# Kernel optimization log

Hardware: AMD Instinct MI355X
Metric: run time of the kernel (lower is better)

Reference implementation:

```python
import jax, jax.numpy as jnp
import numpy as np
from jax import lax

B, S, D, H, W = 4, 4096, 512, 8, 32
LL, LG = 4, 3
HD = D // H
SF = 4   # sparsity_factor
K = 7    # depthwise conv kernel


def _ln(x, g, b):
    mu = x.mean(-1, keepdims=True)
    v = ((x - mu) ** 2).mean(-1, keepdims=True)
    return (x - mu) * lax.rsqrt(v + 1e-5) * g + b


def _mha(x, wqkv, bqkv, wp, bp, bias=None):
    Bx, Sx, Dx = x.shape
    qkv = (x @ wqkv + bqkv).reshape(Bx, Sx, 3, H, HD)
    q, k, v = jnp.moveaxis(qkv, 2, 0)          # each [B,S,H,hd]
    att = jnp.einsum('bqhd,bkhd->bhqk', q, k) * (HD ** -0.5)
    if bias is not None:
        att = att + bias                        # relative position bias [1,H,W,W]
    a = jax.nn.softmax(att, axis=-1)
    o = jnp.einsum('bhqk,bkhd->bqhd', a, v).reshape(Bx, Sx, Dx)
    return o @ wp + bp


def _ffn(x, w1, b1, w2, b2):
    return jax.nn.gelu(x @ w1 + b1) @ w2 + b2


def _dwconv(x, w, b):
    # x [B,S,D], w [D,K] depthwise, 'same' padding
    y = lax.conv_general_dilated(
        x.transpose(0, 2, 1), w[:, None, :], (1,), [((K - 1) // 2, (K - 1) // 2)],
        feature_group_count=D, dimension_numbers=('NCH', 'OIH', 'NCH'))
    return (y + b[:, None]).transpose(0, 2, 1)


def _lin_interp(x, L_out):
    # torch F.interpolate(mode='linear', align_corners=False); x [B,Lin,D]
    Lin = x.shape[1]
    pos = jnp.clip((jnp.arange(L_out, dtype=jnp.float32) + 0.5) * (Lin / L_out) - 0.5,
                   0.0, Lin - 1)
    i0 = jnp.floor(pos).astype(jnp.int32)
    i1 = jnp.minimum(i0 + 1, Lin - 1)
    w = (pos - i0)[None, :, None]
    return x[:, i0] * (1.0 - w) + x[:, i1] * w


_rel_idx = np.arange(W)[:, None] - np.arange(W)[None, :] + W - 1   # [W,W]


def _local_attn(x, wqkv, bqkv, wp, bp, rel):
    # Swin-style non-overlapping window attention with relative position bias
    NW = S // W
    bias = rel[_rel_idx].transpose(2, 0, 1)[None]   # [1,H,W,W]
    xw = x.reshape(B * NW, W, D)
    return _mha(xw, wqkv, bqkv, wp, bp, bias).reshape(B, S, D)


def _global_attn(x, wqkv, bqkv, wp, bp):
    # strided sparse global attention + linear interpolation back to S
    if S > SF * 32:
        stride = max(1, S // (SF * 32))
        xs = x[:, ::stride]                         # [B, 128, D]
        return _lin_interp(_mha(xs, wqkv, bqkv, wp, bp), S)
    return _mha(x, wqkv, bqkv, wp, bp)


def _forward(x, p):
    (lqkv_w, lqkv_b, lproj_w, lproj_b, lrel, lconv_w, lconv_b,
     ln1_g, ln1_b, lffn_w1, lffn_b1, lffn_w2, lffn_b2, ln2_g, ln2_b,
     gqkv_w, gqkv_b, gproj_w, gproj_b, gn1_g, gn1_b,
     gffn_w1, gffn_b1, gffn_w2, gffn_b2, gn2_g, gn2_b,
     fw_local, fw_global, fn_g, fn_b) = p
    # local branch: window attention + depthwise conv + FFN, pre-sum/post-norm
    xl = x
    for i in range(LL):
        a = _local_attn(xl, lqkv_w[i], lqkv_b[i], lproj_w[i], lproj_b[i], lrel[i])
        xl = _ln(xl + a, ln1_g[i], ln1_b[i])
        xl = xl + _dwconv(xl, lconv_w[i], lconv_b[i])
        f = _ffn(xl, lffn_w1[i], lffn_b1[i], lffn_w2[i], lffn_b2[i])
        xl = _ln(xl + f, ln2_g[i], ln2_b[i])
    # global branch: sparse strided attention + FFN
    xg = x
    for i in range(LG):
        a = _global_attn(xg, gqkv_w[i], gqkv_b[i], gproj_w[i], gproj_b[i])
        xg = _ln(xg + a, gn1_g[i], gn1_b[i])
        f = _ffn(xg, gffn_w1[i], gffn_b1[i], gffn_w2[i], gffn_b2[i])
        xg = _ln(xg + f, gn2_g[i], gn2_b[i])
    # weighted_sum branch fusion + LayerNorm
    w = jax.nn.softmax(jnp.stack([fw_local, fw_global]))
    return _ln(w[0] * xl + w[1] * xg, fn_g, fn_b)


def setup_inputs() -> dict:
    ks = iter(jax.random.split(jax.random.key(0), 48))
    def r(shape, s=0.02):
        return jax.random.normal(next(ks), shape, dtype=jnp.float32) * s
    return {
        'x': jax.random.normal(next(ks), (B, S, D), dtype=jnp.float32),
        'lqkv_w': r((LL, D, 3 * D)), 'lqkv_b': jnp.zeros((LL, 3 * D)),
        'lproj_w': r((LL, D, D)), 'lproj_b': jnp.zeros((LL, D)),
        'lrel': r((LL, 2 * W - 1, H)),
        'lconv_w': r((LL, D, K)), 'lconv_b': jnp.zeros((LL, D)),
        'ln1_g': jnp.ones((LL, D)), 'ln1_b': jnp.zeros((LL, D)),
        'lffn_w1': r((LL, D, 4 * D)), 'lffn_b1': jnp.zeros((LL, 4 * D)),
        'lffn_w2': r((LL, 4 * D, D)), 'lffn_b2': jnp.zeros((LL, D)),
        'ln2_g': jnp.ones((LL, D)), 'ln2_b': jnp.zeros((LL, D)),
        'gqkv_w': r((LG, D, 3 * D)), 'gqkv_b': jnp.zeros((LG, 3 * D)),
        'gproj_w': r((LG, D, D)), 'gproj_b': jnp.zeros((LG, D)),
        'gn1_g': jnp.ones((LG, D)), 'gn1_b': jnp.zeros((LG, D)),
        'gffn_w1': r((LG, D, 4 * D)), 'gffn_b1': jnp.zeros((LG, 4 * D)),
        'gffn_w2': r((LG, 4 * D, D)), 'gffn_b2': jnp.zeros((LG, D)),
        'gn2_g': jnp.ones((LG, D)), 'gn2_b': jnp.zeros((LG, D)),
        'fw_local': jnp.float32(0.5), 'fw_global': jnp.float32(0.5),
        'fn_g': jnp.ones((D,)), 'fn_b': jnp.zeros((D,)),
    }


def reference(x, lqkv_w, lqkv_b, lproj_w, lproj_b, lrel, lconv_w, lconv_b,
              ln1_g, ln1_b, lffn_w1, lffn_b1, lffn_w2, lffn_b2, ln2_g, ln2_b,
              gqkv_w, gqkv_b, gproj_w, gproj_b, gn1_g, gn1_b,
              gffn_w1, gffn_b1, gffn_w2, gffn_b2, gn2_g, gn2_b,
              fw_local, fw_global, fn_g, fn_b):
    return _forward(x, (lqkv_w, lqkv_b, lproj_w, lproj_b, lrel, lconv_w, lconv_b,
                        ln1_g, ln1_b, lffn_w1, lffn_b1, lffn_w2, lffn_b2, ln2_g, ln2_b,
                        gqkv_w, gqkv_b, gproj_w, gproj_b, gn1_g, gn1_b,
                        gffn_w1, gffn_b1, gffn_w2, gffn_b2, gn2_g, gn2_b,
                        fw_local, fw_global, fn_g, fn_b))
```

## Files before the change

### kernel.cpp

```cpp
#include <hip/hip_runtime.h>
#include <math.h>

typedef __attribute__((ext_vector_type(8))) short short8;
typedef __attribute__((ext_vector_type(4))) float float4_t;
typedef __attribute__((ext_vector_type(4))) unsigned short ushort4_t;

#define DEV static __device__ __forceinline__

DEV unsigned short f2b(float f) {
    union { float f; unsigned int u; } x; x.f = f;
    unsigned int r = x.u + 0x7fffu + ((x.u >> 16) & 1u);
    return (unsigned short)(r >> 16);
}
DEV float b2f(unsigned short u) {
    union { unsigned int u; float f; } x; x.u = ((unsigned int)u) << 16;
    return x.f;
}
DEV float gelu_f(float x) {
    float u = 0.7978845608028654f * (x + 0.044715f * x * x * x);
    float e = __expf(-2.0f * u);
    return x / (1.0f + e);
}

DEV void gld16(unsigned short* lds, const unsigned short* g) {
    __builtin_amdgcn_global_load_lds(
        (const __attribute__((address_space(1))) unsigned int*)g,
        (__attribute__((address_space(3))) unsigned int*)lds,
        16, 0, 0);
}

__global__ __launch_bounds__(256) void transpose_cast_kernel(
    const float* __restrict__ W, unsigned short* __restrict__ WT, int Kd, int Nd)
{
    __shared__ float tile[32][33];
    int n0 = blockIdx.x * 32, k0 = blockIdx.y * 32;
    int tx = threadIdx.x & 31, ty = threadIdx.x >> 5;
    #pragma unroll
    for (int r = ty; r < 32; r += 8)
        tile[r][tx] = W[(size_t)(k0 + r) * Nd + n0 + tx];
    __syncthreads();
    #pragma unroll
    for (int r = ty; r < 32; r += 8)
        WT[(size_t)(n0 + r) * Kd + k0 + tx] = f2b(tile[tx][r]);
}

__global__ __launch_bounds__(256) void copy_cast_kernel(
    const float* __restrict__ x, float* __restrict__ xl, float* __restrict__ xg,
    unsigned short* __restrict__ xb, int n)
{
    int i = blockIdx.x * 256 + threadIdx.x;
    if (i < n) { float v = x[i]; xl[i] = v; xg[i] = v; xb[i] = f2b(v); }
}

template<int BN>
__global__ __launch_bounds__(256) void gemm_db_kernel(
    const unsigned short* __restrict__ A,
    const unsigned short* __restrict__ BT,
    const float* __restrict__ bias,
    const float* __restrict__ residual,
    float* __restrict__ Cf,
    unsigned short* __restrict__ Cb,
    int M, int N, int K, int act)
{
    constexpr int NI = (BN == 128) ? 4 : 2;
    __shared__ __align__(16) unsigned short As[2][128 * 32];
    __shared__ __align__(16) unsigned short Bs[2][BN * 32];
    const int tid = threadIdx.x;
    const int wave = tid >> 6, lane = tid & 63;
    const int quad = lane >> 4, l16 = lane & 15;
    const int m0 = blockIdx.x * 128, n0 = blockIdx.y * BN;
    const int wm = (BN == 128) ? (wave >> 1) * 64 : wave * 32;
    const int wn = (BN == 128) ? (wave & 1) * 64 : 0;

    float4_t acc[NI][4] = {};

    const int lrow = lane >> 2;
    const int lcol = (lane & 3) * 8;
    const int r0 = wave * 16 + lrow;
    const unsigned short* Ag0 = A  + (size_t)(m0 + r0) * K + lcol;
    const unsigned short* Ag1 = A  + (size_t)(m0 + 64 + r0) * K + lcol;
    const unsigned short* Bg0 = BT + (size_t)(n0 + r0) * K + lcol;
    const unsigned short* Bg1 = (BN == 128) ? BT + (size_t)(n0 + 64 + r0) * K + lcol : nullptr;
    const int soff = (wave * 16) * 32 + lane * 8;

    const int iters = K >> 5;
    gld16(&As[0][soff], Ag0);
    gld16(&As[0][soff + 64 * 32], Ag1);
    gld16(&Bs[0][soff], Bg0);
    if (BN == 128) gld16(&Bs[0][soff + 64 * 32], Bg1);
    __syncthreads();

    for (int k = 0; k < iters; k++) {
        const int cur = k & 1;
        if (k + 1 < iters) {
            const int koff = (k + 1) << 5;
            const int nxt = cur ^ 1;
            gld16(&As[nxt][soff], Ag0 + koff);
            gld16(&As[nxt][soff + 64 * 32], Ag1 + koff);
            gld16(&Bs[nxt][soff], Bg0 + koff);
            if (BN == 128) gld16(&Bs[nxt][soff + 64 * 32], Bg1 + koff);
        }
        short8 a[NI], b[4];
        #pragma unroll
        for (int i = 0; i < NI; i++)
            a[i] = *(const short8*)(&As[cur][(wm + i * 16 + l16) * 32 + quad * 8]);
        #pragma unroll
        for (int j = 0; j < 4; j++)
            b[j] = *(const short8*)(&Bs[cur][(wn + j * 16 + l16) * 32 + quad * 8]);
        #pragma unroll
        for (int i = 0; i < NI; i++)
            #pragma unroll
            for (int j = 0; j < 4; j++)
                acc[i][j] = __builtin_amdgcn_mfma_f32_16x16x32_bf16(b[j], a[i], acc[i][j], 0, 0, 0);
        __syncthreads();
    }

    #pragma unroll
    for (int i = 0; i < NI; i++) {
        const int row = m0 + wm + i * 16 + l16;
        #pragma unroll
        for (int j = 0; j < 4; j++) {
            const int col = n0 + wn + j * 16 + quad * 4;
            const size_t idx = (size_t)row * N + col;
            float4_t v = acc[i][j] + *(const float4_t*)(bias + col);
            if (act == 1) {
                #pragma unroll
                for (int r = 0; r < 4; r++) v[r] = gelu_f(v[r]);
            }
            if (residual) v += *(const float4_t*)(residual + idx);
            if (Cf) *(float4_t*)(Cf + idx) = v;
            if (Cb) {
                ushort4_t o = { f2b(v[0]), f2b(v[1]), f2b(v[2]), f2b(v[3]) };
                *(ushort4_t*)(Cb + idx) = o;
            }
        }
    }
}

__global__ __launch_bounds__(256) void ln_kernel(
    const float* __restrict__ X, const float* __restrict__ g, const float* __restrict__ b,
    float* __restrict__ Yf, unsigned short* __restrict__ Yb)
{
    const int row = blockIdx.x, tid = threadIdx.x;
    const float* xr = X + (size_t)row * 512;
    float v0 = xr[tid], v1 = xr[tid + 256];
    float s = v0 + v1;
    #pragma unroll
    for (int o = 32; o > 0; o >>= 1) s += __shfl_down(s, o);
    __shared__ float red[4];
    __shared__ float stat[2];
    if ((tid & 63) == 0) red[tid >> 6] = s;
    __syncthreads();
    if (tid == 0) stat[0] = (red[0] + red[1] + red[2] + red[3]) * (1.0f / 512.0f);
    __syncthreads();
    float mu = stat[0];
    float d0 = v0 - mu, d1 = v1 - mu;
    float s2 = d0 * d0 + d1 * d1;
    #pragma unroll
    for (int o = 32; o > 0; o >>= 1) s2 += __shfl_down(s2, o);
    if ((tid & 63) == 0) red[tid >> 6] = s2;
    __syncthreads();
    if (tid == 0) stat[1] = rsqrtf((red[0] + red[1] + red[2] + red[3]) * (1.0f / 512.0f) + 1e-5f);
    __syncthreads();
    float rs = stat[1];
    float y0 = d0 * rs * g[tid] + b[tid];
    float y1 = d1 * rs * g[tid + 256] + b[tid + 256];
    if (Yf) { float* yr = Yf + (size_t)row * 512; yr[tid] = y0; yr[tid + 256] = y1; }
    if (Yb) { unsigned short* yb = Yb + (size_t)row * 512; yb[tid] = f2b(y0); yb[tid + 256] = f2b(y1); }
}

__global__ __launch_bounds__(256) void interp_ln_kernel(
    const float* __restrict__ GA, float* __restrict__ XG,
    const float* __restrict__ g, const float* __restrict__ b,
    unsigned short* __restrict__ Yb)
{
    const int row = blockIdx.x, tid = threadIdx.x;
    const int bb = row >> 12, s = row & 4095;
    float pos = (s + 0.5f) * (128.0f / 4096.0f) - 0.5f;
    pos = fminf(fmaxf(pos, 0.0f), 127.0f);
    int i0 = (int)floorf(pos);
    int i1 = min(i0 + 1, 127);
    float w = pos - (float)i0;
    const float* ga0 = GA + ((size_t)bb * 128 + i0) * 512;
    const float* ga1 = GA + ((size_t)bb * 128 + i1) * 512;
    float* xr = XG + (size_t)row * 512;
    float v0 = xr[tid]       + ga0[tid]       * (1.0f - w) + ga1[tid]       * w;
    float v1 = xr[tid + 256] + ga0[tid + 256] * (1.0f - w) + ga1[tid + 256] * w;
    float sm = v0 + v1;
    #pragma unroll
    for (int o = 32; o > 0; o >>= 1) sm += __shfl_down(sm, o);
    __shared__ float red[4];
    __shared__ float stat[2];
    if ((tid & 63) == 0) red[tid >> 6] = sm;
    __syncthreads();
    if (tid == 0) stat[0] = (red[0] + red[1] + red[2] + red[3]) * (1.0f / 512.0f);
    __syncthreads();
    float mu = stat[0];
    float d0 = v0 - mu, d1 = v1 - mu;
    float s2 = d0 * d0 + d1 * d1;
    #pragma unroll
    for (int o = 32; o > 0; o >>= 1) s2 += __shfl_down(s2, o);
    if ((tid & 63) == 0) red[tid >> 6] = s2;
    __syncthreads();
    if (tid == 0) stat[1] = rsqrtf((red[0] + red[1] + red[2] + red[3]) * (1.0f / 512.0f) + 1e-5f);
    __syncthreads();
    float rs = stat[1];
    float y0 = d0 * rs * g[tid] + b[tid];
    float y1 = d1 * rs * g[tid + 256] + b[tid + 256];
    xr[tid] = y0;           xr[tid + 256] = y1;
    unsigned short* yb = Yb + (size_t)row * 512;
    yb[tid] = f2b(y0);      yb[tid + 256] = f2b(y1);
}

__global__ __launch_bounds__(256) void local_attn_kernel(
    const unsigned short* __restrict__ QKV, const float* __restrict__ rel,
    unsigned short* __restrict__ OUT)
{
    const int blk = blockIdx.x;
    const int h = blk & 7;
    const int win = (blk >> 3) & 127;
    const int b = blk >> 10;
    const int rowbase = b * 4096 + win * 32;
    __shared__ float q[32][64], k[32][65], v[32][64];
    __shared__ float sc[32][33];
    const int tid = threadIdx.x;
    for (int idx = tid; idx < 2048; idx += 256) {
        int i = idx >> 6, d = idx & 63;
        const unsigned short* base = QKV + (size_t)(rowbase + i) * 1536 + h * 64 + d;
        q[i][d] = b2f(base[0]);
        k[i][d] = b2f(base[512]);
        v[i][d] = b2f(base[1024]);
    }
    __syncthreads();
    for (int idx = tid; idx < 1024; idx += 256) {
        int i = idx >> 5, j = idx & 31;
        float s = 0.f;
        #pragma unroll
        for (int d = 0; d < 64; d++) s += q[i][d] * k[j][d];
        sc[i][j] = s * 0.125f + rel[(i - j + 31) * 8 + h];
    }
    __syncthreads();
    if (tid < 32) {
        float mx = -1e30f;
        for (int j = 0; j < 32; j++) mx = fmaxf(mx, sc[tid][j]);
        float sum = 0.f;
        for (int j = 0; j < 32; j++) { float e = __expf(sc[tid][j] - mx); sc[tid][j] = e; sum += e; }
        float inv = 1.0f / sum;
        for (int j = 0; j < 32; j++) sc[tid][j] *= inv;
    }
    __syncthreads();
    for (int idx = tid; idx < 2048; idx += 256) {
        int i = idx >> 6, d = idx & 63;
        float o = 0.f;
        #pragma unroll
        for (int j = 0; j < 32; j++) o += sc[i][j] * v[j][d];
        OUT[(size_t)(rowbase + i) * 512 + h * 64 + d] = f2b(o);
    }
}

__global__ __launch_bounds__(256) void gather_xs_kernel(
    const float* __restrict__ XG, unsigned short* __restrict__ XSB)
{
    int i = blockIdx.x * 256 + threadIdx.x;
    if (i < 262144) {
        int d = i & 511, t = (i >> 9) & 127, b = i >> 16;
        XSB[i] = f2b(XG[((size_t)b * 4096 + t * 32) * 512 + d]);
    }
}

__global__ __launch_bounds__(256) void global_attn_kernel(
    const unsigned short* __restrict__ GQKV, unsigned short* __restrict__ GOUT)
{
    const int blk = blockIdx.x;
    const int qt = blk & 3, h = (blk >> 2) & 7, b = blk >> 5;
    __shared__ unsigned short ks[128 * 64], vs[128 * 64];
    __shared__ float qs[32 * 64];
    __shared__ float sc[32 * 128];
    const int tid = threadIdx.x;
    for (int idx = tid; idx < 128 * 64; idx += 256) {
        int j = idx >> 6, d = idx & 63;
        const unsigned short* rowp = GQKV + (size_t)(b * 128 + j) * 1536 + h * 64 + d;
        ks[idx] = rowp[512];
        vs[idx] = rowp[1024];
    }
    for (int idx = tid; idx < 32 * 64; idx += 256) {
        int i = idx >> 6, d = idx & 63;
        qs[idx] = b2f(GQKV[(size_t)(b * 128 + qt * 32 + i) * 1536 + h * 64 + d]);
    }
    __syncthreads();
    for (int idx = tid; idx < 32 * 128; idx += 256) {
        int i = idx >> 7, j = idx & 127;
        float s = 0.f;
        #pragma unroll
        for (int d = 0; d < 64; d++) s += qs[i * 64 + d] * b2f(ks[j * 64 + d]);
        sc[idx] = s * 0.125f;
    }
    __syncthreads();
    if (tid < 32) {
        float mx = -1e30f;
        for (int j = 0; j < 128; j++) mx = fmaxf(mx, sc[tid * 128 + j]);
        float sum = 0.f;
        for (int j = 0; j < 128; j++) { float e = __expf(sc[tid * 128 + j] - mx); sc[tid * 128 + j] = e; sum += e; }
        float inv = 1.0f / sum;
        for (int j = 0; j < 128; j++) sc[tid * 128 + j] *= inv;
    }
    __syncthreads();
    for (int idx = tid; idx < 32 * 64; idx += 256) {
        int i = idx >> 6, d = idx & 63;
        float o = 0.f;
        for (int j = 0; j < 128; j++) o += sc[i * 128 + j] * b2f(vs[j * 64 + d]);
        GOUT[(size_t)(b * 128 + qt * 32 + i) * 512 + h * 64 + d] = f2b(o);
    }
}

__global__ __launch_bounds__(256) void dwconv_add_kernel(
    const float* __restrict__ X, const float* __restrict__ wconv, const float* __restrict__ bconv,
    float* __restrict__ Yf, unsigned short* __restrict__ Yb)
{
    int i = blockIdx.x * 256 + threadIdx.x;
    if (i < 2097152) {
        int dv = (i & 127) * 4;
        int s = (i >> 7) & 4095;
        int b = i >> 19;
        float4_t acc = *(const float4_t*)(bconv + dv);
        #pragma unroll
        for (int t = 0; t < 7; t++) {
            int ss = s + t - 3;
            if (ss >= 0 && ss < 4096) {
                float4_t xv = *(const float4_t*)(X + ((size_t)b * 4096 + ss) * 512 + dv);
                float4_t wv = { wconv[dv * 7 + t], wconv[(dv + 1) * 7 + t],
                                wconv[(dv + 2) * 7 + t], wconv[(dv + 3) * 7 + t] };
                acc += xv * wv;
            }
        }
        size_t e = (size_t)i * 4;
        float4_t v = *(const float4_t*)(X + e) + acc;
        *(float4_t*)(Yf + e) = v;
        ushort4_t o = { f2b(v[0]), f2b(v[1]), f2b(v[2]), f2b(v[3]) };
        *(ushort4_t*)(Yb + e) = o;
    }
}

__global__ __launch_bounds__(256) void final_kernel(
    const float* __restrict__ XL, const float* __restrict__ XG,
    const float* __restrict__ fwl, const float* __restrict__ fwg,
    const float* __restrict__ g, const float* __restrict__ bb, float* __restrict__ out)
{
    const int row = blockIdx.x, tid = threadIdx.x;
    float a = fwl[0], c = fwg[0];
    float m = fmaxf(a, c);
    float ea = __expf(a - m), ec = __expf(c - m);
    float w0 = ea / (ea + ec), w1 = ec / (ea + ec);
    const float* xlr = XL + (size_t)row * 512;
    const float* xgr = XG + (size_t)row * 512;
    float v0 = w0 * xlr[tid] + w1 * xgr[tid];
    float v1 = w0 * xlr[tid + 256] + w1 * xgr[tid + 256];
    float s = v0 + v1;
    #pragma unroll
    for (int o = 32; o > 0; o >>= 1) s += __shfl_down(s, o);
    __shared__ float red[4];
    __shared__ float stat[2];
    if ((tid & 63) == 0) red[tid >> 6] = s;
    __syncthreads();
    if (tid == 0) stat[0] = (red[0] + red[1] + red[2] + red[3]) * (1.0f / 512.0f);
    __syncthreads();
    float mu = stat[0];
    float d0 = v0 - mu, d1 = v1 - mu;
    float s2 = d0 * d0 + d1 * d1;
    #pragma unroll
    for (int o = 32; o > 0; o >>= 1) s2 += __shfl_down(s2, o);
    if ((tid & 63) == 0) red[tid >> 6] = s2;
    __syncthreads();
    if (tid == 0) stat[1] = rsqrtf((red[0] + red[1] + red[2] + red[3]) * (1.0f / 512.0f) + 1e-5f);
    __syncthreads();
    float rs = stat[1];
    float* orow = out + (size_t)row * 512;
    orow[tid]       = d0 * rs * g[tid] + bb[tid];
    orow[tid + 256] = d1 * rs * g[tid + 256] + bb[tid + 256];
}

extern "C" void kernel_launch(void* const* d_in, const int* in_sizes, int n_in,
                              void* d_out, int out_size, void* d_ws, size_t ws_size,
                              hipStream_t stream)
{
    (void)in_sizes; (void)n_in; (void)out_size; (void)ws_size;
    const float* x       = (const float*)d_in[0];
    const float* lqkv_w  = (const float*)d_in[1];
    const float* lqkv_b  = (const float*)d_in[2];
    const float* lproj_w = (const float*)d_in[3];
    const float* lproj_b = (const float*)d_in[4];
    const float* lrel    = (const float*)d_in[5];
    const float* lconv_w = (const float*)d_in[6];
    const float* lconv_b = (const float*)d_in[7];
    const float* ln1_g   = (const float*)d_in[8];
    const float* ln1_b   = (const float*)d_in[9];
    const float* lffn_w1 = (const float*)d_in[10];
    const float* lffn_b1 = (const float*)d_in[11];
    const float* lffn_w2 = (const float*)d_in[12];
    const float* lffn_b2 = (const float*)d_in[13];
    const float* ln2_g   = (const float*)d_in[14];
    const float* ln2_b   = (const float*)d_in[15];
    const float* gqkv_w  = (const float*)d_in[16];
    const float* gqkv_b  = (const float*)d_in[17];
    const float* gproj_w = (const float*)d_in[18];
    const float* gproj_b = (const float*)d_in[19];
    const float* gn1_g   = (const float*)d_in[20];
    const float* gn1_b   = (const float*)d_in[21];
    const float* gffn_w1 = (const float*)d_in[22];
    const float* gffn_b1 = (const float*)d_in[23];
    const float* gffn_w2 = (const float*)d_in[24];
    const float* gffn_b2 = (const float*)d_in[25];
    const float* gn2_g   = (const float*)d_in[26];
    const float* gn2_b   = (const float*)d_in[27];
    const float* fw_local  = (const float*)d_in[28];
    const float* fw_global = (const float*)d_in[29];
    const float* fn_g    = (const float*)d_in[30];
    const float* fn_b    = (const float*)d_in[31];
    float* out = (float*)d_out;

    const int Btot = 4 * 4096;
    const int nel = Btot * 512;

    char* wsb = (char*)d_ws;
    size_t off = 0;
    auto alloc = [&](size_t bytes) -> void* {
        void* p = wsb + off;
        off = (off + bytes + 255) & ~(size_t)255;
        return p;
    };
    float*          XL   = (float*)alloc((size_t)nel * 4);
    float*          XG   = (float*)alloc((size_t)nel * 4);
    float*          TMP  = (float*)alloc((size_t)nel * 4);
    unsigned short* XBl  = (unsigned short*)alloc((size_t)nel * 2);
    unsigned short* XBg  = (unsigned short*)alloc((size_t)nel * 2);
    unsigned short* AOUT = (unsigned short*)alloc((size_t)nel * 2);
    unsigned short* BIG  = (unsigned short*)alloc((size_t)Btot * 2048 * 2);
    unsigned short* WT   = (unsigned short*)alloc((size_t)22020096 * 2);
    unsigned short* XSB  = (unsigned short*)alloc((size_t)512 * 512 * 2);
    unsigned short* GQKV = (unsigned short*)alloc((size_t)512 * 1536 * 2);
    unsigned short* GOUT = (unsigned short*)alloc((size_t)512 * 512 * 2);
    float*          GA   = (float*)alloc((size_t)512 * 512 * 4);

    const size_t perL = 3145728;
    auto transpose = [&](const float* W_, unsigned short* WT_, int Kd, int Nd) {
        dim3 g(Nd / 32, Kd / 32);
        transpose_cast_kernel<<<g, dim3(256), 0, stream>>>(W_, WT_, Kd, Nd);
    };
    for (int i = 0; i < 4; i++) {
        unsigned short* base = WT + (size_t)i * perL;
        transpose(lqkv_w  + (size_t)i * 512 * 1536, base,                         512, 1536);
        transpose(lproj_w + (size_t)i * 512 * 512,  base + 786432,                512, 512);
        transpose(lffn_w1 + (size_t)i * 512 * 2048, base + 786432 + 262144,       512, 2048);
        transpose(lffn_w2 + (size_t)i * 2048 * 512, base + 786432 + 262144 + 1048576, 2048, 512);
    }
    for (int i = 0; i < 3; i++) {
        unsigned short* base = WT + (size_t)(4 + i) * perL;
        transpose(gqkv_w  + (size_t)i * 512 * 1536, base,                         512, 1536);
        transpose(gproj_w + (size_t)i * 512 * 512,  base + 786432,                512, 512);
        transpose(gffn_w1 + (size_t)i * 512 * 2048, base + 786432 + 262144,       512, 2048);
        transpose(gffn_w2 + (size_t)i * 2048 * 512, base + 786432 + 262144 + 1048576, 2048, 512);
    }

    copy_cast_kernel<<<dim3(nel / 256), dim3(256), 0, stream>>>(x, XL, XG, XBl, nel);

    auto gemm = [&](const unsigned short* A_, const unsigned short* BT_, const float* bias_,
                    const float* res_, float* Cf_, unsigned short* Cb_,
                    int M_, int N_, int K_, int act_) {
        if (N_ >= 1024) {
            dim3 g(M_ / 128, N_ / 128);
            gemm_db_kernel<128><<<g, dim3(256), 0, stream>>>(A_, BT_, bias_, res_, Cf_, Cb_, M_, N_, K_, act_);
        } else {
            dim3 g(M_ / 128, N_ / 64);
            gemm_db_kernel<64><<<g, dim3(256), 0, stream>>>(A_, BT_, bias_, res_, Cf_, Cb_, M_, N_, K_, act_);
        }
    };

    for (int i = 0; i < 4; i++) {
        unsigned short* base  = WT + (size_t)i * perL;
        unsigned short* qkvT  = base;
        unsigned short* projT = base + 786432;
        unsigned short* w1T   = base + 786432 + 262144;
        unsigned short* w2T   = base + 786432 + 262144 + 1048576;

        gemm(XBl, qkvT, lqkv_b + i * 1536, nullptr, nullptr, BIG, Btot, 1536, 512, 0);
        local_attn_kernel<<<dim3(4096), dim3(256), 0, stream>>>(BIG, lrel + (size_t)i * 63 * 8, AOUT);
        gemm(AOUT, projT, lproj_b + i * 512, XL, TMP, nullptr, Btot, 512, 512, 0);
        ln_kernel<<<dim3(Btot), dim3(256), 0, stream>>>(TMP, ln1_g + i * 512, ln1_b + i * 512, XL, (unsigned short*)nullptr);
        dwconv_add_kernel<<<dim3(nel / 1024), dim3(256), 0, stream>>>(XL, lconv_w + (size_t)i * 512 * 7, lconv_b + i * 512, TMP, XBl);
        gemm(XBl, w1T, lffn_b1 + i * 2048, nullptr, nullptr, BIG, Btot, 2048, 512, 1);
        gemm(BIG, w2T, lffn_b2 + i * 512, TMP, TMP, nullptr, Btot, 512, 2048, 0);
        ln_kernel<<<dim3(Btot), dim3(256), 0, stream>>>(TMP, ln2_g + i * 512, ln2_b + i * 512, XL, XBl);
    }

    for (int i = 0; i < 3; i++) {
        unsigned short* base  = WT + (size_t)(4 + i) * perL;
        unsigned short* qkvT  = base;
        unsigned short* projT = base + 786432;
        unsigned short* w1T   = base + 786432 + 262144;
        unsigned short* w2T   = base + 786432 + 262144 + 1048576;

        gather_xs_kernel<<<dim3(1024), dim3(256), 0, stream>>>(XG, XSB);
        gemm(XSB, qkvT, gqkv_b + i * 1536, nullptr, nullptr, GQKV, 512, 1536, 512, 0);
        global_attn_kernel<<<dim3(128), dim3(256), 0, stream>>>(GQKV, GOUT);
        gemm(GOUT, projT, gproj_b + i * 512, nullptr, GA, nullptr, 512, 512, 512, 0);
        interp_ln_kernel<<<dim3(Btot), dim3(256), 0, stream>>>(GA, XG, gn1_g + i * 512, gn1_b + i * 512, XBg);
        gemm(XBg, w1T, gffn_b1 + i * 2048, nullptr, nullptr, BIG, Btot, 2048, 512, 1);
        gemm(BIG, w2T, gffn_b2 + i * 512, XG, TMP, nullptr, Btot, 512, 2048, 0);
        ln_kernel<<<dim3(Btot), dim3(256), 0, stream>>>(TMP, gn2_g + i * 512, gn2_b + i * 512, XG, XBg);
    }

    final_kernel<<<dim3(Btot), dim3(256), 0, stream>>>(XL, XG, fw_local, fw_global, fn_g, fn_b, out);
}
```

Baseline: 2.246 ms.

## Vectorize elementwise kernels, wave-per-row layernorm, batch weight transposes, cheaper GELU

LayerNorm, interp-LN and final kernels now process one row per wavefront with float4 loads and shuffle-only reductions, which removes the shared-memory barriers. Copy, gather and all bf16 stores are vectorized with packed bf16x2 conversion. The weight transposes are batched into four launches over a z-dimension instead of 28 separate launches. Local attention is restructured to use vector loads, a per-row shuffle softmax and 8-wide output accumulation. GELU uses an exp2/rcp form, and the GEMM gains an occupancy hint, which could raise register pressure.

```diff
diff --git a/kernel.cpp b/kernel.cpp
--- a/kernel.cpp
+++ b/kernel.cpp
@@ -1,9 +1,11 @@
 #include <hip/hip_runtime.h>
+#include <hip/hip_bf16.h>
 #include <math.h>
 
 typedef __attribute__((ext_vector_type(8))) short short8;
 typedef __attribute__((ext_vector_type(4))) float float4_t;
-typedef __attribute__((ext_vector_type(4))) unsigned short ushort4_t;
+typedef __attribute__((ext_vector_type(4))) unsigned int uint4_t;
+typedef __attribute__((ext_vector_type(2))) unsigned int uint2_t;
 
 #define DEV static __device__ __forceinline__
 
@@ -16,10 +18,17 @@
     union { unsigned int u; float f; } x; x.u = ((unsigned int)u) << 16;
     return x.f;
 }
+DEV unsigned int f2b2(float lo, float hi) {
+    union { __hip_bfloat162 h; unsigned int u; } c;
+    c.h = __float22bfloat162_rn(make_float2(lo, hi));
+    return c.u;
+}
 DEV float gelu_f(float x) {
-    float u = 0.7978845608028654f * (x + 0.044715f * x * x * x);
-    float e = __expf(-2.0f * u);
-    return x / (1.0f + e);
+    const float a = -2.3022082f, b = -0.10294372f;
+    float x2 = x * x;
+    float p = __builtin_fmaf(x2, b, a);
+    float e = __builtin_amdgcn_exp2f(p * x);
+    return x * __builtin_amdgcn_rcpf(1.0f + e);
 }
 
 DEV void gld16(unsigned short* lds, const unsigned short* g) {
@@ -29,9 +38,14 @@
         16, 0, 0);
 }
 
-__global__ __launch_bounds__(256) void transpose_cast_kernel(
-    const float* __restrict__ W, unsigned short* __restrict__ WT, int Kd, int Nd)
-{
+__global__ __launch_bounds__(256) void transpose_cast_batch_kernel(
+    const float* __restrict__ srcL, const float* __restrict__ srcG, int nl,
+    unsigned short* __restrict__ dst0, size_t perL, int Kd, int Nd)
+{
+    const int z = blockIdx.z;
+    const float* W = (z < nl) ? srcL + (size_t)z * Kd * Nd
+                              : srcG + (size_t)(z - nl) * Kd * Nd;
+    unsigned short* WT = dst0 + (size_t)z * perL;
     __shared__ float tile[32][33];
     int n0 = blockIdx.x * 32, k0 = blockIdx.y * 32;
     int tx = threadIdx.x & 31, ty = threadIdx.x >> 5;
@@ -46,14 +60,20 @@
 
 __global__ __launch_bounds__(256) void copy_cast_kernel(
     const float* __restrict__ x, float* __restrict__ xl, float* __restrict__ xg,
-    unsigned short* __restrict__ xb, int n)
+    unsigned short* __restrict__ xb, int n4)
 {
     int i = blockIdx.x * 256 + threadIdx.x;
-    if (i < n) { float v = x[i]; xl[i] = v; xg[i] = v; xb[i] = f2b(v); }
+    if (i < n4) {
+        float4_t v = ((const float4_t*)x)[i];
+        ((float4_t*)xl)[i] = v;
+        ((float4_t*)xg)[i] = v;
+        uint2_t p = { f2b2(v[0], v[1]), f2b2(v[2], v[3]) };
+        ((uint2_t*)xb)[i] = p;
+    }
 }
 
 template<int BN>
-__global__ __launch_bounds__(256) void gemm_db_kernel(
+__global__ __launch_bounds__(256, 3) void gemm_db_kernel(
     const unsigned short* __restrict__ A,
     const unsigned short* __restrict__ BT,
     const float* __restrict__ bias,
@@ -130,8 +150,8 @@
             if (residual) v += *(const float4_t*)(residual + idx);
             if (Cf) *(float4_t*)(Cf + idx) = v;
             if (Cb) {
-                ushort4_t o = { f2b(v[0]), f2b(v[1]), f2b(v[2]), f2b(v[3]) };
-                *(ushort4_t*)(Cb + idx) = o;
+                uint2_t o = { f2b2(v[0], v[1]), f2b2(v[2], v[3]) };
+                *(uint2_t*)(Cb + idx) = o;
             }
         }
     }
@@ -141,32 +161,37 @@
     const float* __restrict__ X, const float* __restrict__ g, const float* __restrict__ b,
     float* __restrict__ Yf, unsigned short* __restrict__ Yb)
 {
-    const int row = blockIdx.x, tid = threadIdx.x;
-    const float* xr = X + (size_t)row * 512;
-    float v0 = xr[tid], v1 = xr[tid + 256];
-    float s = v0 + v1;
-    #pragma unroll
-    for (int o = 32; o > 0; o >>= 1) s += __shfl_down(s, o);
-    __shared__ float red[4];
-    __shared__ float stat[2];
-    if ((tid & 63) == 0) red[tid >> 6] = s;
-    __syncthreads();
-    if (tid == 0) stat[0] = (red[0] + red[1] + red[2] + red[3]) * (1.0f / 512.0f);
-    __syncthreads();
-    float mu = stat[0];
-    float d0 = v0 - mu, d1 = v1 - mu;
-    float s2 = d0 * d0 + d1 * d1;
-    #pragma unroll
-    for (int o = 32; o > 0; o >>= 1) s2 += __shfl_down(s2, o);
-    if ((tid & 63) == 0) red[tid >> 6] = s2;
-    __syncthreads();
-    if (tid == 0) stat[1] = rsqrtf((red[0] + red[1] + red[2] + red[3]) * (1.0f / 512.0f) + 1e-5f);
-    __syncthreads();
-    float rs = stat[1];
-    float y0 = d0 * rs * g[tid] + b[tid];
-    float y1 = d1 * rs * g[tid + 256] + b[tid + 256];
-    if (Yf) { float* yr = Yf + (size_t)row * 512; yr[tid] = y0; yr[tid + 256] = y1; }
-    if (Yb) { unsigned short* yb = Yb + (size_t)row * 512; yb[tid] = f2b(y0); yb[tid + 256] = f2b(y1); }
+    const int row = blockIdx.x * 4 + (threadIdx.x >> 6);
+    const int lane = threadIdx.x & 63;
+    const float* xr = X + (size_t)row * 512 + lane * 8;
+    float4_t v0 = *(const float4_t*)(xr);
+    float4_t v1 = *(const float4_t*)(xr + 4);
+    float s = v0[0] + v0[1] + v0[2] + v0[3] + v1[0] + v1[1] + v1[2] + v1[3];
+    #pragma unroll
+    for (int m = 32; m > 0; m >>= 1) s += __shfl_xor(s, m);
+    float mu = s * (1.0f / 512.0f);
+    float4_t d0 = v0 - mu, d1 = v1 - mu;
+    float s2 = d0[0]*d0[0] + d0[1]*d0[1] + d0[2]*d0[2] + d0[3]*d0[3]
+             + d1[0]*d1[0] + d1[1]*d1[1] + d1[2]*d1[2] + d1[3]*d1[3];
+    #pragma unroll
+    for (int m = 32; m > 0; m >>= 1) s2 += __shfl_xor(s2, m);
+    float rs = rsqrtf(s2 * (1.0f / 512.0f) + 1e-5f);
+    float4_t g0 = *(const float4_t*)(g + lane * 8);
+    float4_t g1 = *(const float4_t*)(g + lane * 8 + 4);
+    float4_t b0 = *(const float4_t*)(b + lane * 8);
+    float4_t b1 = *(const float4_t*)(b + lane * 8 + 4);
+    float4_t y0 = d0 * rs * g0 + b0;
+    float4_t y1 = d1 * rs * g1 + b1;
+    if (Yf) {
+        float* yr = Yf + (size_t)row * 512 + lane * 8;
+        *(float4_t*)(yr) = y0;
+        *(float4_t*)(yr + 4) = y1;
+    }
+    if (Yb) {
+        uint4_t pk = { f2b2(y0[0], y0[1]), f2b2(y0[2], y0[3]),
+                       f2b2(y1[0], y1[1]), f2b2(y1[2], y1[3]) };
+        *(uint4_t*)(Yb + (size_t)row * 512 + lane * 8) = pk;
+    }
 }
 
 __global__ __launch_bounds__(256) void interp_ln_kernel(
@@ -174,42 +199,40 @@
     const float* __restrict__ g, const float* __restrict__ b,
     unsigned short* __restrict__ Yb)
 {
-    const int row = blockIdx.x, tid = threadIdx.x;
-    const int bb = row >> 12, s = row & 4095;
-    float pos = (s + 0.5f) * (128.0f / 4096.0f) - 0.5f;
+    const int row = blockIdx.x * 4 + (threadIdx.x >> 6);
+    const int lane = threadIdx.x & 63;
+    const int bb = row >> 12, sfull = row & 4095;
+    float pos = (sfull + 0.5f) * (128.0f / 4096.0f) - 0.5f;
     pos = fminf(fmaxf(pos, 0.0f), 127.0f);
     int i0 = (int)floorf(pos);
     int i1 = min(i0 + 1, 127);
     float w = pos - (float)i0;
-    const float* ga0 = GA + ((size_t)bb * 128 + i0) * 512;
-    const float* ga1 = GA + ((size_t)bb * 128 + i1) * 512;
-    float* xr = XG + (size_t)row * 512;
-    float v0 = xr[tid]       + ga0[tid]       * (1.0f - w) + ga1[tid]       * w;
-    float v1 = xr[tid + 256] + ga0[tid + 256] * (1.0f - w) + ga1[tid + 256] * w;
-    float sm = v0 + v1;
-    #pragma unroll
-    for (int o = 32; o > 0; o >>= 1) sm += __shfl_down(sm, o);
-    __shared__ float red[4];
-    __shared__ float stat[2];
-    if ((tid & 63) == 0) red[tid >> 6] = sm;
-    __syncthreads();
-    if (tid == 0) stat[0] = (red[0] + red[1] + red[2] + red[3]) * (1.0f / 512.0f);
-    __syncthreads();
-    float mu = stat[0];
-    float d0 = v0 - mu, d1 = v1 - mu;
-    float s2 = d0 * d0 + d1 * d1;
-    #pragma unroll
-    for (int o = 32; o > 0; o >>= 1) s2 += __shfl_down(s2, o);
-    if ((tid & 63) == 0) red[tid >> 6] = s2;
-    __syncthreads();
-    if (tid == 0) stat[1] = rsqrtf((red[0] + red[1] + red[2] + red[3]) * (1.0f / 512.0f) + 1e-5f);
-    __syncthreads();
-    float rs = stat[1];
-    float y0 = d0 * rs * g[tid] + b[tid];
-    float y1 = d1 * rs * g[tid + 256] + b[tid + 256];
-    xr[tid] = y0;           xr[tid + 256] = y1;
-    unsigned short* yb = Yb + (size_t)row * 512;
-    yb[tid] = f2b(y0);      yb[tid + 256] = f2b(y1);
+    const float* ga0 = GA + ((size_t)bb * 128 + i0) * 512 + lane * 8;
+    const float* ga1 = GA + ((size_t)bb * 128 + i1) * 512 + lane * 8;
+    float* xr = XG + (size_t)row * 512 + lane * 8;
+    float4_t v0 = *(const float4_t*)(xr)     + *(const float4_t*)(ga0)     * (1.0f - w) + *(const float4_t*)(ga1)     * w;
+    float4_t v1 = *(const float4_t*)(xr + 4) + *(const float4_t*)(ga0 + 4) * (1.0f - w) + *(const float4_t*)(ga1 + 4) * w;
+    float s = v0[0] + v0[1] + v0[2] + v0[3] + v1[0] + v1[1] + v1[2] + v1[3];
+    #pragma unroll
+    for (int m = 32; m > 0; m >>= 1) s += __shfl_xor(s, m);
+    float mu = s * (1.0f / 512.0f);
+    float4_t d0 = v0 - mu, d1 = v1 - mu;
+    float s2 = d0[0]*d0[0] + d0[1]*d0[1] + d0[2]*d0[2] + d0[3]*d0[3]
+             + d1[0]*d1[0] + d1[1]*d1[1] + d1[2]*d1[2] + d1[3]*d1[3];
+    #pragma unroll
+    for (int m = 32; m > 0; m >>= 1) s2 += __shfl_xor(s2, m);
+    float rs = rsqrtf(s2 * (1.0f / 512.0f) + 1e-5f);
+    float4_t g0 = *(const float4_t*)(g + lane * 8);
+    float4_t g1 = *(const float4_t*)(g + lane * 8 + 4);
+    float4_t b0 = *(const float4_t*)(b + lane * 8);
+    float4_t b1 = *(const float4_t*)(b + lane * 8 + 4);
+    float4_t y0 = d0 * rs * g0 + b0;
+    float4_t y1 = d1 * rs * g1 + b1;
+    *(float4_t*)(xr) = y0;
+    *(float4_t*)(xr + 4) = y1;
+    uint4_t pk = { f2b2(y0[0], y0[1]), f2b2(y0[2], y0[3]),
+                   f2b2(y1[0], y1[1]), f2b2(y1[2], y1[3]) };
+    *(uint4_t*)(Yb + (size_t)row * 512 + lane * 8) = pk;
 }
 
 __global__ __launch_bounds__(256) void local_attn_kernel(
@@ -224,47 +247,64 @@
     __shared__ float q[32][64], k[32][65], v[32][64];
     __shared__ float sc[32][33];
     const int tid = threadIdx.x;
-    for (int idx = tid; idx < 2048; idx += 256) {
-        int i = idx >> 6, d = idx & 63;
-        const unsigned short* base = QKV + (size_t)(rowbase + i) * 1536 + h * 64 + d;
-        q[i][d] = b2f(base[0]);
-        k[i][d] = b2f(base[512]);
-        v[i][d] = b2f(base[1024]);
-    }
-    __syncthreads();
-    for (int idx = tid; idx < 1024; idx += 256) {
-        int i = idx >> 5, j = idx & 31;
+    const int i = tid >> 3, c = tid & 7;
+    {
+        const unsigned short* base = QKV + (size_t)(rowbase + i) * 1536 + h * 64 + c * 8;
+        short8 qv = *(const short8*)(base);
+        short8 kv = *(const short8*)(base + 512);
+        short8 vv = *(const short8*)(base + 1024);
+        #pragma unroll
+        for (int r = 0; r < 8; r++) {
+            q[i][c * 8 + r] = b2f((unsigned short)qv[r]);
+            k[i][c * 8 + r] = b2f((unsigned short)kv[r]);
+            v[i][c * 8 + r] = b2f((unsigned short)vv[r]);
+        }
+    }
+    __syncthreads();
+    #pragma unroll
+    for (int p = 0; p < 4; p++) {
+        int idx = tid + p * 256;
+        int si = idx >> 5, sj = idx & 31;
         float s = 0.f;
         #pragma unroll
-        for (int d = 0; d < 64; d++) s += q[i][d] * k[j][d];
-        sc[i][j] = s * 0.125f + rel[(i - j + 31) * 8 + h];
-    }
-    __syncthreads();
-    if (tid < 32) {
-        float mx = -1e30f;
-        for (int j = 0; j < 32; j++) mx = fmaxf(mx, sc[tid][j]);
-        float sum = 0.f;
-        for (int j = 0; j < 32; j++) { float e = __expf(sc[tid][j] - mx); sc[tid][j] = e; sum += e; }
+        for (int d = 0; d < 64; d++) s += q[si][d] * k[sj][d];
+        sc[si][sj] = s * 0.125f + rel[(si - sj + 31) * 8 + h];
+    }
+    __syncthreads();
+    {
+        const int j0 = c * 4;
+        float a0 = sc[i][j0], a1 = sc[i][j0 + 1], a2 = sc[i][j0 + 2], a3 = sc[i][j0 + 3];
+        float mx = fmaxf(fmaxf(a0, a1), fmaxf(a2, a3));
+        #pragma unroll
+        for (int m = 1; m < 8; m <<= 1) mx = fmaxf(mx, __shfl_xor(mx, m));
+        float e0 = __expf(a0 - mx), e1 = __expf(a1 - mx), e2 = __expf(a2 - mx), e3 = __expf(a3 - mx);
+        float sum = e0 + e1 + e2 + e3;
+        #pragma unroll
+        for (int m = 1; m < 8; m <<= 1) sum += __shfl_xor(sum, m);
         float inv = 1.0f / sum;
-        for (int j = 0; j < 32; j++) sc[tid][j] *= inv;
-    }
-    __syncthreads();
-    for (int idx = tid; idx < 2048; idx += 256) {
-        int i = idx >> 6, d = idx & 63;
-        float o = 0.f;
-        #pragma unroll
-        for (int j = 0; j < 32; j++) o += sc[i][j] * v[j][d];
-        OUT[(size_t)(rowbase + i) * 512 + h * 64 + d] = f2b(o);
-    }
+        sc[i][j0] = e0 * inv; sc[i][j0 + 1] = e1 * inv; sc[i][j0 + 2] = e2 * inv; sc[i][j0 + 3] = e3 * inv;
+    }
+    __syncthreads();
+    float o[8] = {};
+    #pragma unroll
+    for (int j = 0; j < 32; j++) {
+        float a = sc[i][j];
+        #pragma unroll
+        for (int r = 0; r < 8; r++) o[r] += a * v[j][c * 8 + r];
+    }
+    uint4_t pk = { f2b2(o[0], o[1]), f2b2(o[2], o[3]), f2b2(o[4], o[5]), f2b2(o[6], o[7]) };
+    *(uint4_t*)(OUT + (size_t)(rowbase + i) * 512 + h * 64 + c * 8) = pk;
 }
 
 __global__ __launch_bounds__(256) void gather_xs_kernel(
     const float* __restrict__ XG, unsigned short* __restrict__ XSB)
 {
     int i = blockIdx.x * 256 + threadIdx.x;
-    if (i < 262144) {
-        int d = i & 511, t = (i >> 9) & 127, b = i >> 16;
-        XSB[i] = f2b(XG[((size_t)b * 4096 + t * 32) * 512 + d]);
+    if (i < 65536) {
+        int dv = (i & 127) * 4, t = (i >> 7) & 127, b = i >> 14;
+        float4_t v = *(const float4_t*)(XG + ((size_t)b * 4096 + t * 32) * 512 + dv);
+        uint2_t p = { f2b2(v[0], v[1]), f2b2(v[2], v[3]) };
+        *(uint2_t*)(XSB + (size_t)i * 4) = p;
     }
 }
 
@@ -336,8 +376,8 @@
         size_t e = (size_t)i * 4;
         float4_t v = *(const float4_t*)(X + e) + acc;
         *(float4_t*)(Yf + e) = v;
-        ushort4_t o = { f2b(v[0]), f2b(v[1]), f2b(v[2]), f2b(v[3]) };
-        *(ushort4_t*)(Yb + e) = o;
+        uint2_t o = { f2b2(v[0], v[1]), f2b2(v[2], v[3]) };
+        *(uint2_t*)(Yb + e) = o;
     }
 }
 
@@ -346,37 +386,33 @@
     const float* __restrict__ fwl, const float* __restrict__ fwg,
     const float* __restrict__ g, const float* __restrict__ bb, float* __restrict__ out)
 {
-    const int row = blockIdx.x, tid = threadIdx.x;
-    float a = fwl[0], c = fwg[0];
-    float m = fmaxf(a, c);
-    float ea = __expf(a - m), ec = __expf(c - m);
+    const int row = blockIdx.x * 4 + (threadIdx.x >> 6);
+    const int lane = threadIdx.x & 63;
+    float a = fwl[0], cc = fwg[0];
+    float m = fmaxf(a, cc);
+    float ea = __expf(a - m), ec = __expf(cc - m);
     float w0 = ea / (ea + ec), w1 = ec / (ea + ec);
-    const float* xlr = XL + (size_t)row * 512;
-    const float* xgr = XG + (size_t)row * 512;
-    float v0 = w0 * xlr[tid] + w1 * xgr[tid];
-    float v1 = w0 * xlr[tid + 256] + w1 * xgr[tid + 256];
-    float s = v0 + v1;
-    #pragma unroll
-    for (int o = 32; o > 0; o >>= 1) s += __shfl_down(s, o);
-    __shared__ float red[4];
-    __shared__ float stat[2];
-    if ((tid & 63) == 0) red[tid >> 6] = s;
-    __syncthreads();
-    if (tid == 0) stat[0] = (red[0] + red[1] + red[2] + red[3]) * (1.0f / 512.0f);
-    __syncthreads();
-    float mu = stat[0];
-    float d0 = v0 - mu, d1 = v1 - mu;
-    float s2 = d0 * d0 + d1 * d1;
-    #pragma unroll
-    for (int o = 32; o > 0; o >>= 1) s2 += __shfl_down(s2, o);
-    if ((tid & 63) == 0) red[tid >> 6] = s2;
-    __syncthreads();
-    if (tid == 0) stat[1] = rsqrtf((red[0] + red[1] + red[2] + red[3]) * (1.0f / 512.0f) + 1e-5f);
-    __syncthreads();
-    float rs = stat[1];
-    float* orow = out + (size_t)row * 512;
-    orow[tid]       = d0 * rs * g[tid] + bb[tid];
-    orow[tid + 256] = d1 * rs * g[tid + 256] + bb[tid + 256];
+    const float* xlr = XL + (size_t)row * 512 + lane * 8;
+    const float* xgr = XG + (size_t)row * 512 + lane * 8;
+    float4_t v0 = *(const float4_t*)(xlr)     * w0 + *(const float4_t*)(xgr)     * w1;
+    float4_t v1 = *(const float4_t*)(xlr + 4) * w0 + *(const float4_t*)(xgr + 4) * w1;
+    float s = v0[0] + v0[1] + v0[2] + v0[3] + v1[0] + v1[1] + v1[2] + v1[3];
+    #pragma unroll
+    for (int mm = 32; mm > 0; mm >>= 1) s += __shfl_xor(s, mm);
+    float mu = s * (1.0f / 512.0f);
+    float4_t d0 = v0 - mu, d1 = v1 - mu;
+    float s2 = d0[0]*d0[0] + d0[1]*d0[1] + d0[2]*d0[2] + d0[3]*d0[3]
+             + d1[0]*d1[0] + d1[1]*d1[1] + d1[2]*d1[2] + d1[3]*d1[3];
+    #pragma unroll
+    for (int mm = 32; mm > 0; mm >>= 1) s2 += __shfl_xor(s2, mm);
+    float rs = rsqrtf(s2 * (1.0f / 512.0f) + 1e-5f);
+    float4_t g0 = *(const float4_t*)(g + lane * 8);
+    float4_t g1 = *(const float4_t*)(g + lane * 8 + 4);
+    float4_t b0 = *(const float4_t*)(bb + lane * 8);
+    float4_t b1 = *(const float4_t*)(bb + lane * 8 + 4);
+    float* orow = out + (size_t)row * 512 + lane * 8;
+    *(float4_t*)(orow)     = d0 * rs * g0 + b0;
+    *(float4_t*)(orow + 4) = d1 * rs * g1 + b1;
 }
 
 extern "C" void kernel_launch(void* const* d_in, const int* in_sizes, int n_in,
@@ -442,26 +478,19 @@
     float*          GA   = (float*)alloc((size_t)512 * 512 * 4);
 
     const size_t perL = 3145728;
-    auto transpose = [&](const float* W_, unsigned short* WT_, int Kd, int Nd) {
-        dim3 g(Nd / 32, Kd / 32);
-        transpose_cast_kernel<<<g, dim3(256), 0, stream>>>(W_, WT_, Kd, Nd);
-    };
-    for (int i = 0; i < 4; i++) {
-        unsigned short* base = WT + (size_t)i * perL;
-        transpose(lqkv_w  + (size_t)i * 512 * 1536, base,                         512, 1536);
-        transpose(lproj_w + (size_t)i * 512 * 512,  base + 786432,                512, 512);
-        transpose(lffn_w1 + (size_t)i * 512 * 2048, base + 786432 + 262144,       512, 2048);
-        transpose(lffn_w2 + (size_t)i * 2048 * 512, base + 786432 + 262144 + 1048576, 2048, 512);
-    }
-    for (int i = 0; i < 3; i++) {
-        unsigned short* base = WT + (size_t)(4 + i) * perL;
-        transpose(gqkv_w  + (size_t)i * 512 * 1536, base,                         512, 1536);
-        transpose(gproj_w + (size_t)i * 512 * 512,  base + 786432,                512, 512);
-        transpose(gffn_w1 + (size_t)i * 512 * 2048, base + 786432 + 262144,       512, 2048);
-        transpose(gffn_w2 + (size_t)i * 2048 * 512, base + 786432 + 262144 + 1048576, 2048, 512);
-    }
-
-    copy_cast_kernel<<<dim3(nel / 256), dim3(256), 0, stream>>>(x, XL, XG, XBl, nel);
+    {
+        dim3 blk(256);
+        transpose_cast_batch_kernel<<<dim3(1536/32, 512/32, 7), blk, 0, stream>>>(
+            lqkv_w, gqkv_w, 4, WT, perL, 512, 1536);
+        transpose_cast_batch_kernel<<<dim3(512/32, 512/32, 7), blk, 0, stream>>>(
+            lproj_w, gproj_w, 4, WT + 786432, perL, 512, 512);
+        transpose_cast_batch_kernel<<<dim3(2048/32, 512/32, 7), blk, 0, stream>>>(
+            lffn_w1, gffn_w1, 4, WT + 786432 + 262144, perL, 512, 2048);
+        transpose_cast_batch_kernel<<<dim3(512/32, 2048/32, 7), blk, 0, stream>>>(
+            lffn_w2, gffn_w2, 4, WT + 786432 + 262144 + 1048576, perL, 2048, 512);
+    }
+
+    copy_cast_kernel<<<dim3(nel / 1024), dim3(256), 0, stream>>>(x, XL, XG, XBl, nel / 4);
 
     auto gemm = [&](const unsigned short* A_, const unsigned short* BT_, const float* bias_,
                     const float* res_, float* Cf_, unsigned short* Cb_,
@@ -485,11 +514,11 @@
         gemm(XBl, qkvT, lqkv_b + i * 1536, nullptr, nullptr, BIG, Btot, 1536, 512, 0);
         local_attn_kernel<<<dim3(4096), dim3(256), 0, stream>>>(BIG, lrel + (size_t)i * 63 * 8, AOUT);
         gemm(AOUT, projT, lproj_b + i * 512, XL, TMP, nullptr, Btot, 512, 512, 0);
-        ln_kernel<<<dim3(Btot), dim3(256), 0, stream>>>(TMP, ln1_g + i * 512, ln1_b + i * 512, XL, (unsigned short*)nullptr);
+        ln_kernel<<<dim3(Btot / 4), dim3(256), 0, stream>>>(TMP, ln1_g + i * 512, ln1_b + i * 512, XL, (unsigned short*)nullptr);
         dwconv_add_kernel<<<dim3(nel / 1024), dim3(256), 0, stream>>>(XL, lconv_w + (size_t)i * 512 * 7, lconv_b + i * 512, TMP, XBl);
         gemm(XBl, w1T, lffn_b1 + i * 2048, nullptr, nullptr, BIG, Btot, 2048, 512, 1);
         gemm(BIG, w2T, lffn_b2 + i * 512, TMP, TMP, nullptr, Btot, 512, 2048, 0);
-        ln_kernel<<<dim3(Btot), dim3(256), 0, stream>>>(TMP, ln2_g + i * 512, ln2_b + i * 512, XL, XBl);
+        ln_kernel<<<dim3(Btot / 4), dim3(256), 0, stream>>>(TMP, ln2_g + i * 512, ln2_b + i * 512, XL, XBl);
     }
 
     for (int i = 0; i < 3; i++) {
@@ -499,15 +528,15 @@
         unsigned short* w1T   = base + 786432 + 262144;
         unsigned short* w2T   = base + 786432 + 262144 + 1048576;
 
-        gather_xs_kernel<<<dim3(1024), dim3(256), 0, stream>>>(XG, XSB);
+        gather_xs_kernel<<<dim3(256), dim3(256), 0, stream>>>(XG, XSB);
         gemm(XSB, qkvT, gqkv_b + i * 1536, nullptr, nullptr, GQKV, 512, 1536, 512, 0);
         global_attn_kernel<<<dim3(128), dim3(256), 0, stream>>>(GQKV, GOUT);
         gemm(GOUT, projT, gproj_b + i * 512, nullptr, GA, nullptr, 512, 512, 512, 0);
-        interp_ln_kernel<<<dim3(Btot), dim3(256), 0, stream>>>(GA, XG, gn1_g + i * 512, gn1_b + i * 512, XBg);
+        interp_ln_kernel<<<dim3(Btot / 4), dim3(256), 0, stream>>>(GA, XG, gn1_g + i * 512, gn1_b + i * 512, XBg);
         gemm(XBg, w1T, gffn_b1 + i * 2048, nullptr, nullptr, BIG, Btot, 2048, 512, 1);
         gemm(BIG, w2T, gffn_b2 + i * 512, XG, TMP, nullptr, Btot, 512, 2048, 0);
-        ln_kernel<<<dim3(Btot), dim3(256), 0, stream>>>(TMP, gn2_g + i * 512, gn2_b + i * 512, XG, XBg);
-    }
-
-    final_kernel<<<dim3(Btot), dim3(256), 0, stream>>>(XL, XG, fw_local, fw_global, fn_g, fn_b, out);
-}
+        ln_kernel<<<dim3(Btot / 4), dim3(256), 0, stream>>>(TMP, gn2_g + i * 512, gn2_b + i * 512, XG, XBg);
+    }
+
+    final_kernel<<<dim3(Btot / 4), dim3(256), 0, stream>>>(XL, XG, fw_local, fw_global, fn_g, fn_b, out);
+}
```

After: 2.062 ms. 8.2% less time.
